# Kernel tuning notes

Measured on AMD Instinct MI355X. Metric: run time of the kernel, lower is better.

The kernel has to match this reference:

```python
import jax, jax.numpy as jnp
import numpy as np

B, L, D = 16, 2048, 192  # batch, frames_per_data, units
H, K = 4, 12             # num_heads, key_dim (hardcoded in build())
EPS = 1e-3               # keras LayerNormalization default epsilon


def layer_norm(x, g, b):
    m = jnp.mean(x, axis=-1, keepdims=True)
    v = jnp.mean(jnp.square(x - m), axis=-1, keepdims=True)
    return (x - m) * jax.lax.rsqrt(v + EPS) * g + b


def conv1d_valid(x, w, b):
    # x: [B,L,C], w: [3,Cin,Cout] -> [B,L-2,Cout]
    return jax.lax.conv_general_dilated(
        x, w, window_strides=(1,), padding='VALID',
        dimension_numbers=('NWC', 'WIO', 'NWC')) + b


def setup_inputs() -> dict:
    key = jax.random.key(0)
    ks = jax.random.split(key, 16)
    s = 0.05
    return {
        'x': jax.random.normal(ks[0], (B, L, D), jnp.float32),
        'ln1_g': jnp.ones((D,), jnp.float32),
        'ln1_b': jnp.zeros((D,), jnp.float32),
        'wq': jax.random.normal(ks[1], (D, H, K), jnp.float32) * s,
        'bq': jnp.zeros((H, K), jnp.float32),
        'wk': jax.random.normal(ks[2], (D, H, K), jnp.float32) * s,
        'bk': jnp.zeros((H, K), jnp.float32),
        'wv': jax.random.normal(ks[3], (D, H, K), jnp.float32) * s,
        'bv': jnp.zeros((H, K), jnp.float32),
        'wo': jax.random.normal(ks[4], (H, K, D), jnp.float32) * s,
        'bo': jnp.zeros((D,), jnp.float32),
        'ln2_g': jnp.ones((D,), jnp.float32),
        'ln2_b': jnp.zeros((D,), jnp.float32),
        'c1_w': jax.random.normal(ks[5], (3, D, D), jnp.float32) * s,
        'c1_b': jnp.zeros((D,), jnp.float32),
        'c2_w': jax.random.normal(ks[6], (3, D, D), jnp.float32) * s,
        'c2_b': jnp.zeros((D,), jnp.float32),
    }


def reference(x, ln1_g, ln1_b, wq, bq, wk, bk, wv, bv, wo, bo,
              ln2_g, ln2_b, c1_w, c1_b, c2_w, c2_b):
    # --- LN1 + causal MHA + residual (dropout = identity at inference) ---
    xn = layer_norm(x, ln1_g, ln1_b)
    q = jnp.einsum('bld,dhk->blhk', xn, wq) + bq
    k = jnp.einsum('bld,dhk->blhk', xn, wk) + bk
    v = jnp.einsum('bld,dhk->blhk', xn, wv) + bv
    scores = jnp.einsum('blhk,bmhk->bhlm', q, k) / jnp.sqrt(jnp.float32(K))
    causal = jnp.tril(jnp.ones((L, L), jnp.float32))  # tril(True) mask
    scores = scores + (1.0 - causal) * (-1e9)          # keras additive mask
    attn = jax.nn.softmax(scores, axis=-1)
    ctx = jnp.einsum('bhlm,bmhk->blhk', attn, v)
    mha = jnp.einsum('blhk,hkd->bld', ctx, wo) + bo
    x = x + mha
    # --- LN2 + positionwise Conv1D feedforward + residual ---
    xn = layer_norm(x, ln2_g, ln2_b)
    h = jax.nn.relu(conv1d_valid(xn, c1_w, c1_b))      # [B,L-2,D]
    h = jnp.pad(h, ((0, 0), (1, 1), (0, 0)))           # ZeroPadding1D(1,1)
    h = conv1d_valid(h, c2_w, c2_b)                    # [B,L-2,D]
    h = jnp.pad(h, ((0, 0), (1, 1), (0, 0)))
    return x + h
```

## Files before the change

### kernel.cpp

```cpp
#include <hip/hip_runtime.h>
#include <hip/hip_bf16.h>

#define L_ 2048
#define D_ 192
#define HK_ 48
#define EPS_ 1e-3f
#define SCALE_ 0.28867513459481287f

typedef __hip_bfloat16 bf16;
typedef _Float16 f16;
typedef __fp16 hf16x2 __attribute__((ext_vector_type(2)));
typedef _Float16 f16x4 __attribute__((ext_vector_type(4)));
typedef __bf16 bf16x8 __attribute__((ext_vector_type(8)));
typedef float  f32x4  __attribute__((ext_vector_type(4)));

__device__ __forceinline__ float b2f(bf16 x) { return __bfloat162float(x); }
__device__ __forceinline__ bf16 f2b(float x) { return __float2bfloat16(x); }

__global__ __launch_bounds__(256) void k_prep_all(
    const float* __restrict__ c1w, const float* __restrict__ c2w,
    const float* __restrict__ wq, const float* __restrict__ wk, const float* __restrict__ wv,
    const float* __restrict__ bq, const float* __restrict__ bk, const float* __restrict__ bv,
    const float* __restrict__ wo,
    bf16* __restrict__ wrep1, bf16* __restrict__ wrep2,
    bf16* __restrict__ wrepq, float* __restrict__ bias144, bf16* __restrict__ wrepo)
{
    const int i = blockIdx.x * 256 + threadIdx.x;
    if (i < 110592) {
        const int k = i / 192, n = i - k * 192;
        wrep1[((size_t)(k >> 5) * 192 + n) * 32 + (k & 31)] = f2b(c1w[i]);
    } else if (i < 221184) {
        const int j = i - 110592;
        const int k = j / 192, n = j - k * 192;
        wrep2[((size_t)(k >> 5) * 192 + n) * 32 + (k & 31)] = f2b(c2w[j]);
    } else if (i < 248832) {
        const int j = i - 221184;
        const int kb = j / 4608, rem = j % 4608;
        const int n = rem / 32, kk = rem % 32;
        const int k = kb * 32 + kk;
        float v;
        if (n < 48)       v = wq[k * HK_ + n] * SCALE_;
        else if (n < 96)  v = wk[k * HK_ + (n - 48)];
        else              v = wv[k * HK_ + (n - 96)];
        wrepq[j] = f2b(v);
    } else if (i < 248976) {
        const int j = i - 248832;
        bias144[j] = (j < 48) ? bq[j] * SCALE_
                   : (j < 96) ? bk[j - 48] : bv[j - 96];
    } else if (i < 261264) {
        const int j = i - 248976;
        const int kb = j / 6144, rem = j % 6144;
        const int n = rem / 32, kk = rem % 32;
        const int k = kb * 32 + kk;
        wrepo[j] = f2b(k < 48 ? wo[k * D_ + n] : 0.f);
    }
}

__global__ __launch_bounds__(256) void k_ln_qkv(
    const float* __restrict__ x, const float* __restrict__ g1, const float* __restrict__ b1,
    const bf16* __restrict__ wrep, const float* __restrict__ bias144,
    f16* __restrict__ qo, f16* __restrict__ ko, f16* __restrict__ vt)
{
    __shared__ bf16 xn[64 * 200];
    const int tid = threadIdx.x;
    const int wave = tid >> 6, lane = tid & 63;
    const int rowbase = blockIdx.x * 64;
    const int b = rowbase >> 11;
    const int lrow0 = rowbase & 2047;

    const float gg0 = g1[lane], gg1 = g1[lane + 64], gg2 = g1[lane + 128];
    const float bb0 = b1[lane], bb1 = b1[lane + 64], bb2 = b1[lane + 128];
    for (int i = 0; i < 16; ++i) {
        const int r = wave * 16 + i;
        const float* xp = x + (size_t)(rowbase + r) * D_;
        const float x0 = xp[lane];
        const float x1 = xp[lane + 64];
        const float x2 = xp[lane + 128];
        float s = x0 + x1 + x2;
        float q = x0 * x0 + x1 * x1 + x2 * x2;
        #pragma unroll
        for (int m = 1; m < 64; m <<= 1) {
            s += __shfl_xor(s, m, 64);
            q += __shfl_xor(q, m, 64);
        }
        const float mean = s * (1.0f / 192.0f);
        const float var  = q * (1.0f / 192.0f) - mean * mean;
        const float rs   = rsqrtf(var + EPS_);
        xn[r * 200 + lane]       = f2b((x0 - mean) * rs * gg0 + bb0);
        xn[r * 200 + lane + 64]  = f2b((x1 - mean) * rs * gg1 + bb1);
        xn[r * 200 + lane + 128] = f2b((x2 - mean) * rs * gg2 + bb2);
    }

    {
        const int h  = tid >> 6;
        const int vc = 12 + ((tid >> 4) & 3);
        const int p0 = lrow0 + (tid & 15) * 4;
        f16x4 vv;
        vv[0] = vv[1] = vv[2] = vv[3] = (vc == 12) ? (f16)1.0f : (f16)0.0f;
        *(f16x4*)(vt + ((size_t)(b * 4 + h) * 16 + vc) * 2048 + p0) = vv;
    }
    __syncthreads();

    const int l15 = lane & 15, q4 = lane >> 4;
    f32x4 acc[9];
    #pragma unroll
    for (int nt = 0; nt < 9; ++nt) acc[nt] = (f32x4){0.f, 0.f, 0.f, 0.f};

    const bf16* xrow = xn + (wave * 16 + l15) * 200 + q4 * 8;
    #pragma unroll
    for (int kb = 0; kb < 6; ++kb) {
        const bf16x8 a = *(const bf16x8*)(xrow + kb * 32);
        const bf16* wp = wrep + ((size_t)kb * 144 + l15) * 32 + q4 * 8;
        #pragma unroll
        for (int nt = 0; nt < 9; ++nt) {
            const bf16x8 bfr = *(const bf16x8*)(wp + (size_t)nt * 16 * 32);
            acc[nt] = __builtin_amdgcn_mfma_f32_16x16x32_bf16(a, bfr, acc[nt], 0, 0, 0);
        }
    }

    const int rw = rowbase + wave * 16 + q4 * 4;
    #pragma unroll
    for (int nt = 0; nt < 9; ++nt) {
        const int col = nt * 16 + l15;
        const float bd = bias144[col];
        if (nt < 3) {
            #pragma unroll
            for (int reg = 0; reg < 4; ++reg)
                qo[(size_t)(rw + reg) * HK_ + col] = (f16)(acc[nt][reg] + bd);
        } else if (nt < 6) {
            #pragma unroll
            for (int reg = 0; reg < 4; ++reg)
                ko[(size_t)(rw + reg) * HK_ + (col - 48)] = (f16)(acc[nt][reg] + bd);
        } else {
            const int vcol = col - 96;
            const int h = vcol / 12, c12 = vcol % 12;
            f16x4 vv;
            #pragma unroll
            for (int reg = 0; reg < 4; ++reg) vv[reg] = (f16)(acc[nt][reg] + bd);
            *(f16x4*)(vt + ((size_t)(b * 4 + h) * 16 + c12) * 2048 +
                      lrow0 + wave * 16 + q4 * 4) = vv;
        }
    }
}

__global__ __launch_bounds__(256) void k_attn_part(
    const f16* __restrict__ qh, const f16* __restrict__ kh, const f16* __restrict__ vt,
    bf16* __restrict__ part_o, float* __restrict__ part_l)
{
    const int tid = threadIdx.x;
    const int wv = tid >> 6, lane = tid & 63;
    const int quad = lane >> 4, l15 = lane & 15;
    const int bh = blockIdx.x / 36;
    int r = blockIdx.x % 36;
    int qt = 0;
    while (r >= qt + 1) { r -= qt + 1; ++qt; }
    const int ks = r;
    const int b = bh >> 2, h = bh & 3;
    const size_t base  = (size_t)b * L_ * HK_ + h * 12;
    const size_t vbase = ((size_t)bh * 16 + l15) * 2048;
    const int kbase = ks * 256;
    const int qbase = qt * 256 + wv * 64;
    const bool diag = (ks == qt);
    const int ktmax = diag ? 4 * (wv + 1) : 16;

    f16x4 Qf[4];
    #pragma unroll
    for (int s = 0; s < 4; ++s) {
        f16x4 v;
        if (quad < 3)
            v = *(const f16x4*)(qh + base + (size_t)(qbase + s * 16 + l15) * HK_ + quad * 4);
        else { v[0] = (f16)1.0f; v[1] = 0; v[2] = 0; v[3] = 0; }
        Qf[s] = v;
    }

    f32x4 O[4];
    #pragma unroll
    for (int s = 0; s < 4; ++s) O[s] = (f32x4){0.f, 0.f, 0.f, 0.f};

    for (int g = 0; g < ktmax; g += 4) {
        f16x4 Kg[4], Vg[4];
        #pragma unroll
        for (int u = 0; u < 4; ++u) {
            const int kt = g + u;
            f16x4 kf;
            if (quad < 3)
                kf = *(const f16x4*)(kh + base + (size_t)(kbase + kt * 16 + l15) * HK_ + quad * 4);
            else { kf[0] = (f16)-6.0f; kf[1] = 0; kf[2] = 0; kf[3] = 0; }
            Kg[u] = kf;
            Vg[u] = *(const f16x4*)(vt + vbase + kbase + kt * 16 + quad * 4);
        }
        #pragma unroll
        for (int u = 0; u < 4; ++u) {
            const int k0 = kbase + (g + u) * 16 + quad * 4;
            #pragma unroll
            for (int s = 0; s < 4; ++s) {
                f32x4 sc = (f32x4){0.f, 0.f, 0.f, 0.f};
                sc = __builtin_amdgcn_mfma_f32_16x16x16f16(Kg[u], Qf[s], sc, 0, 0, 0);
                float p0 = __expf(sc[0]), p1 = __expf(sc[1]);
                float p2 = __expf(sc[2]), p3 = __expf(sc[3]);
                if (diag) {
                    const int qg = qbase + s * 16 + l15;
                    p0 = (k0 + 0 <= qg) ? p0 : 0.f;
                    p1 = (k0 + 1 <= qg) ? p1 : 0.f;
                    p2 = (k0 + 2 <= qg) ? p2 : 0.f;
                    p3 = (k0 + 3 <= qg) ? p3 : 0.f;
                }
                const hf16x2 lo = __builtin_amdgcn_cvt_pkrtz(p0, p1);
                const hf16x2 hi = __builtin_amdgcn_cvt_pkrtz(p2, p3);
                f16x4 p;
                p[0] = (f16)lo[0]; p[1] = (f16)lo[1];
                p[2] = (f16)hi[0]; p[3] = (f16)hi[1];
                O[s] = __builtin_amdgcn_mfma_f32_16x16x16f16(p, Vg[u], O[s], 0, 0, 0);
            }
        }
    }

    const size_t pobase = (size_t)(bh * 8 + ks) * 2048;
    #pragma unroll
    for (int s = 0; s < 4; ++s) {
        const int q16 = qbase + s * 16;
        #pragma unroll
        for (int j = 0; j < 4; ++j) {
            const int qq = q16 + quad * 4 + j;
            if (l15 < 12)       part_o[(pobase + qq) * 12 + l15] = f2b(O[s][j]);
            else if (l15 == 12) part_l[pobase + qq] = O[s][j];
        }
    }
}

__global__ __launch_bounds__(256) void k_proj_ln2(
    const float* __restrict__ x, const bf16* __restrict__ part_o,
    const float* __restrict__ part_l, const bf16* __restrict__ wrepo,
    const float* __restrict__ bo, const float* __restrict__ g2,
    const float* __restrict__ lb2, bf16* __restrict__ x2b,
    bf16* __restrict__ xn2b)
{
    __shared__ bf16 ct[64 * 72];
    const int tid = threadIdx.x;
    const int wave = tid >> 6, lane = tid & 63;
    const int rowbase = blockIdx.x * 64;
    const int b = rowbase >> 11, lrow = rowbase & 2047;
    const int ns = (lrow >> 8) + 1;

    {
        const int rr = tid >> 2, h = tid & 3;
        const int q = lrow + rr;
        const bf16* op = part_o + ((size_t)(b * 4 + h) * 8 * 2048 + q) * 12;
        const float* lp = part_l + (size_t)(b * 4 + h) * 8 * 2048 + q;
        float o[12];
        #pragma unroll
        for (int i = 0; i < 12; ++i) o[i] = 0.f;
        float l = 0.f;
        for (int s = 0; s < ns; ++s) {
            l += lp[(size_t)s * 2048];
            #pragma unroll
            for (int i = 0; i < 12; ++i) o[i] += b2f(op[(size_t)s * 2048 * 12 + i]);
        }
        const float inv = 1.0f / l;
        #pragma unroll
        for (int i = 0; i < 12; ++i) ct[rr * 72 + h * 12 + i] = f2b(o[i] * inv);
        const int c0 = 48 + h * 4;
        #pragma unroll
        for (int i = 0; i < 4; ++i) ct[rr * 72 + c0 + i] = f2b(0.f);
    }
    __syncthreads();

    const int l15 = lane & 15, q4 = lane >> 4;
    f32x4 acc[12];
    #pragma unroll
    for (int nt = 0; nt < 12; ++nt) acc[nt] = (f32x4){0.f, 0.f, 0.f, 0.f};
    const bf16* arow = ct + (wave * 16 + l15) * 72 + q4 * 8;
    #pragma unroll
    for (int kb = 0; kb < 2; ++kb) {
        const bf16x8 a = *(const bf16x8*)(arow + kb * 32);
        const bf16* wp = wrepo + ((size_t)kb * 192 + l15) * 32 + q4 * 8;
        #pragma unroll
        for (int nt = 0; nt < 12; ++nt) {
            const bf16x8 bb = *(const bf16x8*)(wp + (size_t)nt * 16 * 32);
            acc[nt] = __builtin_amdgcn_mfma_f32_16x16x32_bf16(a, bb, acc[nt], 0, 0, 0);
        }
    }

    const int rw0 = rowbase + wave * 16 + q4 * 4;
    float sum[4] = {0.f, 0.f, 0.f, 0.f}, ssum[4] = {0.f, 0.f, 0.f, 0.f};
    #pragma unroll
    for (int nt = 0; nt < 12; ++nt) {
        const int col = nt * 16 + l15;
        const float bod = bo[col];
        #pragma unroll
        for (int reg = 0; reg < 4; ++reg) {
            const float v = acc[nt][reg] + bod + x[(size_t)(rw0 + reg) * D_ + col];
            acc[nt][reg] = v;
            x2b[(size_t)(rw0 + reg) * D_ + col] = f2b(v);
            sum[reg] += v; ssum[reg] += v * v;
        }
    }
    #pragma unroll
    for (int m = 1; m <= 8; m <<= 1) {
        #pragma unroll
        for (int reg = 0; reg < 4; ++reg) {
            sum[reg]  += __shfl_xor(sum[reg], m, 64);
            ssum[reg] += __shfl_xor(ssum[reg], m, 64);
        }
    }
    float mean[4], rs[4];
    #pragma unroll
    for (int reg = 0; reg < 4; ++reg) {
        mean[reg] = sum[reg] * (1.0f / 192.0f);
        const float var = ssum[reg] * (1.0f / 192.0f) - mean[reg] * mean[reg];
        rs[reg] = rsqrtf(var + EPS_);
    }
    #pragma unroll
    for (int nt = 0; nt < 12; ++nt) {
        const int col = nt * 16 + l15;
        const float g = g2[col], bb2 = lb2[col];
        #pragma unroll
        for (int reg = 0; reg < 4; ++reg)
            xn2b[(size_t)(rw0 + reg) * D_ + col] =
                f2b((acc[nt][reg] - mean[reg]) * rs[reg] * g + bb2);
    }
}

#define INROWB 400
#define HTOFF  27200
__global__ __launch_bounds__(256, 2) void k_conv_fused(
    const bf16* __restrict__ act, const bf16* __restrict__ w1,
    const float* __restrict__ b1c, const bf16* __restrict__ w2,
    const float* __restrict__ b2c, const bf16* __restrict__ x2b,
    float* __restrict__ outf)
{
    __shared__ __align__(16) char lds[27200 + 26400];

    const int tid = threadIdx.x;
    const int wave = tid >> 6, lane = tid & 63;
    const int m16 = lane & 15, q = lane >> 4;
    const int rowbase = blockIdx.x * 64;
    const int lrow = rowbase & (L_ - 1);

    {
        const bf16* src0 = act + ((long long)rowbase - 2) * D_;
        bf16x8 v[7];
        int dst[7];
        #pragma unroll
        for (int i = 0; i < 7; ++i) {
            const int g = tid + i * 256;
            if (g < 1632) {
                v[i] = *(const bf16x8*)(src0 + g * 8);
                const int row = (g * 2731) >> 16;
                dst[i] = row * INROWB + (g - row * 24) * 16;
            }
        }
        #pragma unroll
        for (int i = 0; i < 7; ++i) {
            const int g = tid + i * 256;
            if (g < 1632) *(bf16x8*)(lds + dst[i]) = v[i];
        }
    }

    const int laneA = m16 * INROWB + q * 16;
    const int colw = wave * 48;
    float bd1[3], bd2[3];
    #pragma unroll
    for (int j = 0; j < 3; ++j) {
        bd1[j] = b1c[colw + j * 16 + m16];
        bd2[j] = b2c[colw + j * 16 + m16];
    }
    __syncthreads();

    f32x4 acc1[5][3];
    #pragma unroll
    for (int mt = 0; mt < 5; ++mt)
        #pragma unroll
        for (int j = 0; j < 3; ++j) acc1[mt][j] = (f32x4){0.f, 0.f, 0.f, 0.f};

    #define LOADB(w, kb, j) \
        (*(const bf16x8*)((w) + ((size_t)(kb) * 192 + m16) * 32 + q * 8 \
                          + (size_t)(wave * 3 + (j)) * 16 * 32))
    {
        bf16x8 bB[2][3];
        #pragma unroll
        for (int j = 0; j < 3; ++j) bB[0][j] = LOADB(w1, 0, j);
        #pragma unroll
        for (int kb = 0; kb < 18; ++kb) {
            if (kb + 1 < 18) {
                #pragma unroll
                for (int j = 0; j < 3; ++j) bB[(kb + 1) & 1][j] = LOADB(w1, kb + 1, j);
            }
            const int t = kb / 6, c6 = kb % 6;
            bf16x8 a[5];
            #pragma unroll
            for (int mt = 0; mt < 5; ++mt)
                a[mt] = *(const bf16x8*)(lds + laneA + (mt * 16 + t) * INROWB + c6 * 64);
            #pragma unroll
            for (int j = 0; j < 3; ++j)
                #pragma unroll
                for (int mt = 0; mt < 5; ++mt)
                    acc1[mt][j] = __builtin_amdgcn_mfma_f32_16x16x32_bf16(
                        a[mt], bB[kb & 1][j], acc1[mt][j], 0, 0, 0);
        }
    }

    #pragma unroll
    for (int mt = 0; mt < 5; ++mt)
        #pragma unroll
        for (int j = 0; j < 3; ++j)
            #pragma unroll
            for (int reg = 0; reg < 4; ++reg) {
                const int hr = mt * 16 + q * 4 + reg;
                if (hr < 66) {
                    const int hm = lrow + hr - 1;
                    float v = fmaxf(acc1[mt][j][reg] + bd1[j], 0.f);
                    if (hm == 0 || hm == L_ - 1) v = 0.f;
                    *(bf16*)(lds + HTOFF + hr * INROWB + (colw + j * 16 + m16) * 2) = f2b(v);
                }
            }
    __syncthreads();

    float xr[3][4][4];
    #pragma unroll
    for (int j = 0; j < 3; ++j)
        #pragma unroll
        for (int mt = 0; mt < 4; ++mt)
            #pragma unroll
            for (int reg = 0; reg < 4; ++reg)
                xr[j][mt][reg] = b2f(x2b[(size_t)(rowbase + mt * 16 + q * 4 + reg) * D_
                                         + colw + j * 16 + m16]);

    f32x4 acc2[4][3];
    #pragma unroll
    for (int mt = 0; mt < 4; ++mt)
        #pragma unroll
        for (int j = 0; j < 3; ++j) acc2[mt][j] = (f32x4){0.f, 0.f, 0.f, 0.f};
    {
        bf16x8 bB[2][3];
        #pragma unroll
        for (int j = 0; j < 3; ++j) bB[0][j] = LOADB(w2, 0, j);
        #pragma unroll
        for (int kb = 0; kb < 18; ++kb) {
            if (kb + 1 < 18) {
                #pragma unroll
                for (int j = 0; j < 3; ++j) bB[(kb + 1) & 1][j] = LOADB(w2, kb + 1, j);
            }
            const int t = kb / 6, c6 = kb % 6;
            bf16x8 a[4];
            #pragma unroll
            for (int mt = 0; mt < 4; ++mt)
                a[mt] = *(const bf16x8*)(lds + HTOFF + laneA + (mt * 16 + t) * INROWB + c6 * 64);
            #pragma unroll
            for (int j = 0; j < 3; ++j)
                #pragma unroll
                for (int mt = 0; mt < 4; ++mt)
                    acc2[mt][j] = __builtin_amdgcn_mfma_f32_16x16x32_bf16(
                        a[mt], bB[kb & 1][j], acc2[mt][j], 0, 0, 0);
        }
    }
    #undef LOADB

    #pragma unroll
    for (int j = 0; j < 3; ++j)
        #pragma unroll
        for (int mt = 0; mt < 4; ++mt)
            #pragma unroll
            for (int reg = 0; reg < 4; ++reg) {
                const int r = rowbase + mt * 16 + q * 4 + reg;
                const int m = r & (L_ - 1);
                float v = xr[j][mt][reg];
                if (m != 0 && m != L_ - 1) v += acc2[mt][j][reg] + bd2[j];
                outf[(size_t)r * D_ + colw + j * 16 + m16] = v;
            }
}

extern "C" void kernel_launch(void* const* d_in, const int* in_sizes, int n_in,
                              void* d_out, int out_size, void* d_ws, size_t ws_size,
                              hipStream_t stream)
{
    const float* x    = (const float*)d_in[0];
    const float* ln1g = (const float*)d_in[1];
    const float* ln1b = (const float*)d_in[2];
    const float* wq   = (const float*)d_in[3];
    const float* bq   = (const float*)d_in[4];
    const float* wk   = (const float*)d_in[5];
    const float* bk   = (const float*)d_in[6];
    const float* wv   = (const float*)d_in[7];
    const float* bv   = (const float*)d_in[8];
    const float* wo   = (const float*)d_in[9];
    const float* bo   = (const float*)d_in[10];
    const float* ln2g = (const float*)d_in[11];
    const float* ln2b = (const float*)d_in[12];
    const float* c1w  = (const float*)d_in[13];
    const float* c1b  = (const float*)d_in[14];
    const float* c2w  = (const float*)d_in[15];
    const float* c2b  = (const float*)d_in[16];

    const size_t ROWS = (size_t)16 * L_;
    char* ws = (char*)d_ws;
    size_t off = 4096;
    bf16* xn2b = (bf16*)(ws + off); off += ROWS * D_ * 2;
    off += 4096;
    bf16* hpb  = (bf16*)(ws + off); off += ROWS * D_ * 2;
    off += 4096;
    bf16* x2b  = (bf16*)(ws + off); off += ROWS * D_ * 2;
    f16* qb    = (f16*)(ws + off);   off += ROWS * HK_ * 2;
    f16* kb    = (f16*)(ws + off);   off += ROWS * HK_ * 2;
    f16* vt    = (f16*)(ws + off);   off += (size_t)64 * 16 * 2048 * 2;
    bf16* part_o = (bf16*)(ws + off); off += (size_t)64 * 8 * 2048 * 12 * 2;
    float* part_l = (float*)(ws + off); off += (size_t)64 * 8 * 2048 * 4;
    bf16* wrep1 = (bf16*)(ws + off); off += 576 * 192 * 2;
    bf16* wrep2 = (bf16*)(ws + off); off += 576 * 192 * 2;
    bf16* wrepq = (bf16*)(ws + off); off += 6 * 144 * 32 * 2;
    float* bias144 = (float*)(ws + off); off += 144 * 4;
    bf16* wrepo = (bf16*)(ws + off); off += 2 * 192 * 32 * 2;

    (void)hpb;
    k_prep_all   <<<1021, 256, 0, stream>>>(c1w, c2w, wq, wk, wv, bq, bk, bv, wo,
                                            wrep1, wrep2, wrepq, bias144, wrepo);
    k_ln_qkv     <<< 512, 256, 0, stream>>>(x, ln1g, ln1b, wrepq, bias144, qb, kb, vt);
    k_attn_part  <<<64 * 36, 256, 0, stream>>>(qb, kb, vt, part_o, part_l);
    k_proj_ln2   <<< 512, 256, 0, stream>>>(x, part_o, part_l, wrepo, bo, ln2g, ln2b,
                                            x2b, xn2b);
    k_conv_fused <<< 512, 256, 0, stream>>>(xn2b, wrep1, c1b, wrep2, c2b, x2b,
                                            (float*)d_out);
}
```

Measured before the change: 202.1 us.

## Halve row tiles per block, split columns across waves, use exp2 in attention

The LN/QKV, projection+LN2 and fused conv kernels now process 32 rows per block instead of 64 and launch twice as many blocks. Where needed, waves split the output columns, and LN2 partial sums are combined through shared memory. Attention folds log2(e) into the Q scaling and the shift term so it can call the hardware exp2 directly, and its K-tile unroll drops from 4 to 2, with higher launch-bound occupancy hints. The aim is more parallelism and occupancy across the 256 CUs, at the cost of more conv halo recompute (36 input rows per 32 outputs) and an extra block barrier.

Measured after the change: 194.3 us. -3.9%, faster.

```diff
diff --git a/kernel.cpp b/kernel.cpp
--- a/kernel.cpp
+++ b/kernel.cpp
@@ -6,6 +6,7 @@
 #define HK_ 48
 #define EPS_ 1e-3f
 #define SCALE_ 0.28867513459481287f
+#define LOG2E_ 1.4426950408889634f
 
 typedef __hip_bfloat16 bf16;
 typedef _Float16 f16;
@@ -39,13 +40,13 @@
         const int n = rem / 32, kk = rem % 32;
         const int k = kb * 32 + kk;
         float v;
-        if (n < 48)       v = wq[k * HK_ + n] * SCALE_;
+        if (n < 48)       v = wq[k * HK_ + n] * (SCALE_ * LOG2E_);
         else if (n < 96)  v = wk[k * HK_ + (n - 48)];
         else              v = wv[k * HK_ + (n - 96)];
         wrepq[j] = f2b(v);
     } else if (i < 248976) {
         const int j = i - 248832;
-        bias144[j] = (j < 48) ? bq[j] * SCALE_
+        bias144[j] = (j < 48) ? bq[j] * (SCALE_ * LOG2E_)
                    : (j < 96) ? bk[j - 48] : bv[j - 96];
     } else if (i < 261264) {
         const int j = i - 248976;
@@ -56,22 +57,22 @@
     }
 }
 
-__global__ __launch_bounds__(256) void k_ln_qkv(
+__global__ __launch_bounds__(256, 4) void k_ln_qkv(
     const float* __restrict__ x, const float* __restrict__ g1, const float* __restrict__ b1,
     const bf16* __restrict__ wrep, const float* __restrict__ bias144,
     f16* __restrict__ qo, f16* __restrict__ ko, f16* __restrict__ vt)
 {
-    __shared__ bf16 xn[64 * 200];
+    __shared__ bf16 xn[32 * 200];
     const int tid = threadIdx.x;
     const int wave = tid >> 6, lane = tid & 63;
-    const int rowbase = blockIdx.x * 64;
+    const int rowbase = blockIdx.x * 32;
     const int b = rowbase >> 11;
     const int lrow0 = rowbase & 2047;
 
     const float gg0 = g1[lane], gg1 = g1[lane + 64], gg2 = g1[lane + 128];
     const float bb0 = b1[lane], bb1 = b1[lane + 64], bb2 = b1[lane + 128];
-    for (int i = 0; i < 16; ++i) {
-        const int r = wave * 16 + i;
+    for (int i = 0; i < 8; ++i) {
+        const int r = wave * 8 + i;
         const float* xp = x + (size_t)(rowbase + r) * D_;
         const float x0 = xp[lane];
         const float x1 = xp[lane + 64];
@@ -91,10 +92,10 @@
         xn[r * 200 + lane + 128] = f2b((x2 - mean) * rs * gg2 + bb2);
     }
 
-    {
-        const int h  = tid >> 6;
-        const int vc = 12 + ((tid >> 4) & 3);
-        const int p0 = lrow0 + (tid & 15) * 4;
+    if (tid < 128) {
+        const int h  = tid >> 5;
+        const int vc = 12 + ((tid >> 3) & 3);
+        const int p0 = lrow0 + (tid & 7) * 4;
         f16x4 vv;
         vv[0] = vv[1] = vv[2] = vv[3] = (vc == 12) ? (f16)1.0f : (f16)0.0f;
         *(f16x4*)(vt + ((size_t)(b * 4 + h) * 16 + vc) * 2048 + p0) = vv;
@@ -102,48 +103,56 @@
     __syncthreads();
 
     const int l15 = lane & 15, q4 = lane >> 4;
-    f32x4 acc[9];
-    #pragma unroll
-    for (int nt = 0; nt < 9; ++nt) acc[nt] = (f32x4){0.f, 0.f, 0.f, 0.f};
-
-    const bf16* xrow = xn + (wave * 16 + l15) * 200 + q4 * 8;
+    const int rt = wave >> 1, g = wave & 1;
+    const int ntlim = 5 - g;
+    f32x4 acc[5];
+    #pragma unroll
+    for (int nt = 0; nt < 5; ++nt) acc[nt] = (f32x4){0.f, 0.f, 0.f, 0.f};
+
+    const bf16* xrow = xn + (rt * 16 + l15) * 200 + q4 * 8;
     #pragma unroll
     for (int kb = 0; kb < 6; ++kb) {
         const bf16x8 a = *(const bf16x8*)(xrow + kb * 32);
-        const bf16* wp = wrep + ((size_t)kb * 144 + l15) * 32 + q4 * 8;
-        #pragma unroll
-        for (int nt = 0; nt < 9; ++nt) {
-            const bf16x8 bfr = *(const bf16x8*)(wp + (size_t)nt * 16 * 32);
-            acc[nt] = __builtin_amdgcn_mfma_f32_16x16x32_bf16(a, bfr, acc[nt], 0, 0, 0);
-        }
-    }
-
-    const int rw = rowbase + wave * 16 + q4 * 4;
-    #pragma unroll
-    for (int nt = 0; nt < 9; ++nt) {
-        const int col = nt * 16 + l15;
-        const float bd = bias144[col];
-        if (nt < 3) {
-            #pragma unroll
-            for (int reg = 0; reg < 4; ++reg)
-                qo[(size_t)(rw + reg) * HK_ + col] = (f16)(acc[nt][reg] + bd);
-        } else if (nt < 6) {
-            #pragma unroll
-            for (int reg = 0; reg < 4; ++reg)
-                ko[(size_t)(rw + reg) * HK_ + (col - 48)] = (f16)(acc[nt][reg] + bd);
-        } else {
-            const int vcol = col - 96;
-            const int h = vcol / 12, c12 = vcol % 12;
-            f16x4 vv;
-            #pragma unroll
-            for (int reg = 0; reg < 4; ++reg) vv[reg] = (f16)(acc[nt][reg] + bd);
-            *(f16x4*)(vt + ((size_t)(b * 4 + h) * 16 + c12) * 2048 +
-                      lrow0 + wave * 16 + q4 * 4) = vv;
+        const bf16* wp = wrep + ((size_t)kb * 144 + l15) * 32 + q4 * 8
+                       + (size_t)(g * 5) * 16 * 32;
+        #pragma unroll
+        for (int nt = 0; nt < 5; ++nt) {
+            if (nt < ntlim) {
+                const bf16x8 bfr = *(const bf16x8*)(wp + (size_t)nt * 16 * 32);
+                acc[nt] = __builtin_amdgcn_mfma_f32_16x16x32_bf16(a, bfr, acc[nt], 0, 0, 0);
+            }
+        }
+    }
+
+    const int rw = rowbase + rt * 16 + q4 * 4;
+    #pragma unroll
+    for (int nt = 0; nt < 5; ++nt) {
+        if (nt < ntlim) {
+            const int ntg = g * 5 + nt;
+            const int col = ntg * 16 + l15;
+            const float bd = bias144[col];
+            if (ntg < 3) {
+                #pragma unroll
+                for (int reg = 0; reg < 4; ++reg)
+                    qo[(size_t)(rw + reg) * HK_ + col] = (f16)(acc[nt][reg] + bd);
+            } else if (ntg < 6) {
+                #pragma unroll
+                for (int reg = 0; reg < 4; ++reg)
+                    ko[(size_t)(rw + reg) * HK_ + (col - 48)] = (f16)(acc[nt][reg] + bd);
+            } else {
+                const int vcol = col - 96;
+                const int h = vcol / 12, c12 = vcol % 12;
+                f16x4 vv;
+                #pragma unroll
+                for (int reg = 0; reg < 4; ++reg) vv[reg] = (f16)(acc[nt][reg] + bd);
+                *(f16x4*)(vt + ((size_t)(b * 4 + h) * 16 + c12) * 2048 +
+                          lrow0 + rt * 16 + q4 * 4) = vv;
+            }
         }
     }
 }
 
-__global__ __launch_bounds__(256) void k_attn_part(
+__global__ __launch_bounds__(256, 8) void k_attn_part(
     const f16* __restrict__ qh, const f16* __restrict__ kh, const f16* __restrict__ vt,
     bf16* __restrict__ part_o, float* __restrict__ part_l)
 {
@@ -169,7 +178,7 @@
         f16x4 v;
         if (quad < 3)
             v = *(const f16x4*)(qh + base + (size_t)(qbase + s * 16 + l15) * HK_ + quad * 4);
-        else { v[0] = (f16)1.0f; v[1] = 0; v[2] = 0; v[3] = 0; }
+        else { v[0] = (f16)LOG2E_; v[1] = 0; v[2] = 0; v[3] = 0; }
         Qf[s] = v;
     }
 
@@ -177,10 +186,10 @@
     #pragma unroll
     for (int s = 0; s < 4; ++s) O[s] = (f32x4){0.f, 0.f, 0.f, 0.f};
 
-    for (int g = 0; g < ktmax; g += 4) {
-        f16x4 Kg[4], Vg[4];
-        #pragma unroll
-        for (int u = 0; u < 4; ++u) {
+    for (int g = 0; g < ktmax; g += 2) {
+        f16x4 Kg[2], Vg[2];
+        #pragma unroll
+        for (int u = 0; u < 2; ++u) {
             const int kt = g + u;
             f16x4 kf;
             if (quad < 3)
@@ -190,14 +199,16 @@
             Vg[u] = *(const f16x4*)(vt + vbase + kbase + kt * 16 + quad * 4);
         }
         #pragma unroll
-        for (int u = 0; u < 4; ++u) {
+        for (int u = 0; u < 2; ++u) {
             const int k0 = kbase + (g + u) * 16 + quad * 4;
             #pragma unroll
             for (int s = 0; s < 4; ++s) {
                 f32x4 sc = (f32x4){0.f, 0.f, 0.f, 0.f};
                 sc = __builtin_amdgcn_mfma_f32_16x16x16f16(Kg[u], Qf[s], sc, 0, 0, 0);
-                float p0 = __expf(sc[0]), p1 = __expf(sc[1]);
-                float p2 = __expf(sc[2]), p3 = __expf(sc[3]);
+                float p0 = __builtin_amdgcn_exp2f(sc[0]);
+                float p1 = __builtin_amdgcn_exp2f(sc[1]);
+                float p2 = __builtin_amdgcn_exp2f(sc[2]);
+                float p3 = __builtin_amdgcn_exp2f(sc[3]);
                 if (diag) {
                     const int qg = qbase + s * 16 + l15;
                     p0 = (k0 + 0 <= qg) ? p0 : 0.f;
@@ -228,21 +239,22 @@
     }
 }
 
-__global__ __launch_bounds__(256) void k_proj_ln2(
+__global__ __launch_bounds__(256, 4) void k_proj_ln2(
     const float* __restrict__ x, const bf16* __restrict__ part_o,
     const float* __restrict__ part_l, const bf16* __restrict__ wrepo,
     const float* __restrict__ bo, const float* __restrict__ g2,
     const float* __restrict__ lb2, bf16* __restrict__ x2b,
     bf16* __restrict__ xn2b)
 {
-    __shared__ bf16 ct[64 * 72];
+    __shared__ bf16 ct[32 * 72];
+    __shared__ float psum[4][4][4][2];
     const int tid = threadIdx.x;
     const int wave = tid >> 6, lane = tid & 63;
-    const int rowbase = blockIdx.x * 64;
+    const int rowbase = blockIdx.x * 32;
     const int b = rowbase >> 11, lrow = rowbase & 2047;
     const int ns = (lrow >> 8) + 1;
 
-    {
+    if (tid < 128) {
         const int rr = tid >> 2, h = tid & 3;
         const int q = lrow + rr;
         const bf16* op = part_o + ((size_t)(b * 4 + h) * 8 * 2048 + q) * 12;
@@ -266,31 +278,33 @@
     __syncthreads();
 
     const int l15 = lane & 15, q4 = lane >> 4;
-    f32x4 acc[12];
-    #pragma unroll
-    for (int nt = 0; nt < 12; ++nt) acc[nt] = (f32x4){0.f, 0.f, 0.f, 0.f};
-    const bf16* arow = ct + (wave * 16 + l15) * 72 + q4 * 8;
+    const int rt = wave >> 1, g = wave & 1;
+    f32x4 acc[6];
+    #pragma unroll
+    for (int j = 0; j < 6; ++j) acc[j] = (f32x4){0.f, 0.f, 0.f, 0.f};
+    const bf16* arow = ct + (rt * 16 + l15) * 72 + q4 * 8;
     #pragma unroll
     for (int kb = 0; kb < 2; ++kb) {
         const bf16x8 a = *(const bf16x8*)(arow + kb * 32);
-        const bf16* wp = wrepo + ((size_t)kb * 192 + l15) * 32 + q4 * 8;
-        #pragma unroll
-        for (int nt = 0; nt < 12; ++nt) {
-            const bf16x8 bb = *(const bf16x8*)(wp + (size_t)nt * 16 * 32);
-            acc[nt] = __builtin_amdgcn_mfma_f32_16x16x32_bf16(a, bb, acc[nt], 0, 0, 0);
-        }
-    }
-
-    const int rw0 = rowbase + wave * 16 + q4 * 4;
+        const bf16* wp = wrepo + ((size_t)kb * 192 + l15) * 32 + q4 * 8
+                       + (size_t)(g * 6) * 16 * 32;
+        #pragma unroll
+        for (int j = 0; j < 6; ++j) {
+            const bf16x8 bb = *(const bf16x8*)(wp + (size_t)j * 16 * 32);
+            acc[j] = __builtin_amdgcn_mfma_f32_16x16x32_bf16(a, bb, acc[j], 0, 0, 0);
+        }
+    }
+
+    const int rw0 = rowbase + rt * 16 + q4 * 4;
     float sum[4] = {0.f, 0.f, 0.f, 0.f}, ssum[4] = {0.f, 0.f, 0.f, 0.f};
     #pragma unroll
-    for (int nt = 0; nt < 12; ++nt) {
-        const int col = nt * 16 + l15;
+    for (int j = 0; j < 6; ++j) {
+        const int col = (g * 6 + j) * 16 + l15;
         const float bod = bo[col];
         #pragma unroll
         for (int reg = 0; reg < 4; ++reg) {
-            const float v = acc[nt][reg] + bod + x[(size_t)(rw0 + reg) * D_ + col];
-            acc[nt][reg] = v;
+            const float v = acc[j][reg] + bod + x[(size_t)(rw0 + reg) * D_ + col];
+            acc[j][reg] = v;
             x2b[(size_t)(rw0 + reg) * D_ + col] = f2b(v);
             sum[reg] += v; ssum[reg] += v * v;
         }
@@ -303,57 +317,69 @@
             ssum[reg] += __shfl_xor(ssum[reg], m, 64);
         }
     }
+    if (l15 == 0) {
+        #pragma unroll
+        for (int reg = 0; reg < 4; ++reg) {
+            psum[wave][q4][reg][0] = sum[reg];
+            psum[wave][q4][reg][1] = ssum[reg];
+        }
+    }
+    __syncthreads();
     float mean[4], rs[4];
     #pragma unroll
     for (int reg = 0; reg < 4; ++reg) {
-        mean[reg] = sum[reg] * (1.0f / 192.0f);
-        const float var = ssum[reg] * (1.0f / 192.0f) - mean[reg] * mean[reg];
+        const float st = sum[reg]  + psum[wave ^ 1][q4][reg][0];
+        const float qt2 = ssum[reg] + psum[wave ^ 1][q4][reg][1];
+        mean[reg] = st * (1.0f / 192.0f);
+        const float var = qt2 * (1.0f / 192.0f) - mean[reg] * mean[reg];
         rs[reg] = rsqrtf(var + EPS_);
     }
     #pragma unroll
-    for (int nt = 0; nt < 12; ++nt) {
-        const int col = nt * 16 + l15;
-        const float g = g2[col], bb2 = lb2[col];
+    for (int j = 0; j < 6; ++j) {
+        const int col = (g * 6 + j) * 16 + l15;
+        const float gg = g2[col], bb2 = lb2[col];
         #pragma unroll
         for (int reg = 0; reg < 4; ++reg)
             xn2b[(size_t)(rw0 + reg) * D_ + col] =
-                f2b((acc[nt][reg] - mean[reg]) * rs[reg] * g + bb2);
+                f2b((acc[j][reg] - mean[reg]) * rs[reg] * gg + bb2);
     }
 }
 
 #define INROWB 400
-#define HTOFF  27200
-__global__ __launch_bounds__(256, 2) void k_conv_fused(
+#define NIN    36
+#define NH     34
+#define HTOFF  (NIN * INROWB)
+__global__ __launch_bounds__(256, 4) void k_conv_fused(
     const bf16* __restrict__ act, const bf16* __restrict__ w1,
     const float* __restrict__ b1c, const bf16* __restrict__ w2,
     const float* __restrict__ b2c, const bf16* __restrict__ x2b,
     float* __restrict__ outf)
 {
-    __shared__ __align__(16) char lds[27200 + 26400];
+    __shared__ __align__(16) char lds[NIN * INROWB + NH * INROWB];
 
     const int tid = threadIdx.x;
     const int wave = tid >> 6, lane = tid & 63;
     const int m16 = lane & 15, q = lane >> 4;
-    const int rowbase = blockIdx.x * 64;
+    const int rowbase = blockIdx.x * 32;
     const int lrow = rowbase & (L_ - 1);
 
     {
         const bf16* src0 = act + ((long long)rowbase - 2) * D_;
-        bf16x8 v[7];
-        int dst[7];
-        #pragma unroll
-        for (int i = 0; i < 7; ++i) {
+        bf16x8 v[4];
+        int dst[4];
+        #pragma unroll
+        for (int i = 0; i < 4; ++i) {
             const int g = tid + i * 256;
-            if (g < 1632) {
+            if (g < 864) {
                 v[i] = *(const bf16x8*)(src0 + g * 8);
                 const int row = (g * 2731) >> 16;
                 dst[i] = row * INROWB + (g - row * 24) * 16;
             }
         }
         #pragma unroll
-        for (int i = 0; i < 7; ++i) {
+        for (int i = 0; i < 4; ++i) {
             const int g = tid + i * 256;
-            if (g < 1632) *(bf16x8*)(lds + dst[i]) = v[i];
+            if (g < 864) *(bf16x8*)(lds + dst[i]) = v[i];
         }
     }
 
@@ -367,9 +393,9 @@
     }
     __syncthreads();
 
-    f32x4 acc1[5][3];
-    #pragma unroll
-    for (int mt = 0; mt < 5; ++mt)
+    f32x4 acc1[3][3];
+    #pragma unroll
+    for (int mt = 0; mt < 3; ++mt)
         #pragma unroll
         for (int j = 0; j < 3; ++j) acc1[mt][j] = (f32x4){0.f, 0.f, 0.f, 0.f};
 
@@ -387,48 +413,48 @@
                 for (int j = 0; j < 3; ++j) bB[(kb + 1) & 1][j] = LOADB(w1, kb + 1, j);
             }
             const int t = kb / 6, c6 = kb % 6;
-            bf16x8 a[5];
-            #pragma unroll
-            for (int mt = 0; mt < 5; ++mt)
+            bf16x8 a[3];
+            #pragma unroll
+            for (int mt = 0; mt < 3; ++mt)
                 a[mt] = *(const bf16x8*)(lds + laneA + (mt * 16 + t) * INROWB + c6 * 64);
             #pragma unroll
             for (int j = 0; j < 3; ++j)
                 #pragma unroll
-                for (int mt = 0; mt < 5; ++mt)
+                for (int mt = 0; mt < 3; ++mt)
                     acc1[mt][j] = __builtin_amdgcn_mfma_f32_16x16x32_bf16(
                         a[mt], bB[kb & 1][j], acc1[mt][j], 0, 0, 0);
         }
     }
 
     #pragma unroll
-    for (int mt = 0; mt < 5; ++mt)
+    for (int mt = 0; mt < 3; ++mt)
         #pragma unroll
         for (int j = 0; j < 3; ++j)
             #pragma unroll
             for (int reg = 0; reg < 4; ++reg) {
                 const int hr = mt * 16 + q * 4 + reg;
-                if (hr < 66) {
+                if (hr < NH) {
                     const int hm = lrow + hr - 1;
                     float v = fmaxf(acc1[mt][j][reg] + bd1[j], 0.f);
                     if (hm == 0 || hm == L_ - 1) v = 0.f;
                     *(bf16*)(lds + HTOFF + hr * INROWB + (colw + j * 16 + m16) * 2) = f2b(v);
                 }
             }
-    __syncthreads();
-
-    float xr[3][4][4];
+
+    float xr[3][2][4];
     #pragma unroll
     for (int j = 0; j < 3; ++j)
         #pragma unroll
-        for (int mt = 0; mt < 4; ++mt)
+        for (int mt = 0; mt < 2; ++mt)
             #pragma unroll
             for (int reg = 0; reg < 4; ++reg)
                 xr[j][mt][reg] = b2f(x2b[(size_t)(rowbase + mt * 16 + q * 4 + reg) * D_
                                          + colw + j * 16 + m16]);
-
-    f32x4 acc2[4][3];
-    #pragma unroll
-    for (int mt = 0; mt < 4; ++mt)
+    __syncthreads();
+
+    f32x4 acc2[2][3];
+    #pragma unroll
+    for (int mt = 0; mt < 2; ++mt)
         #pragma unroll
         for (int j = 0; j < 3; ++j) acc2[mt][j] = (f32x4){0.f, 0.f, 0.f, 0.f};
     {
@@ -442,14 +468,14 @@
                 for (int j = 0; j < 3; ++j) bB[(kb + 1) & 1][j] = LOADB(w2, kb + 1, j);
             }
             const int t = kb / 6, c6 = kb % 6;
-            bf16x8 a[4];
-            #pragma unroll
-            for (int mt = 0; mt < 4; ++mt)
+            bf16x8 a[2];
+            #pragma unroll
+            for (int mt = 0; mt < 2; ++mt)
                 a[mt] = *(const bf16x8*)(lds + HTOFF + laneA + (mt * 16 + t) * INROWB + c6 * 64);
             #pragma unroll
             for (int j = 0; j < 3; ++j)
                 #pragma unroll
-                for (int mt = 0; mt < 4; ++mt)
+                for (int mt = 0; mt < 2; ++mt)
                     acc2[mt][j] = __builtin_amdgcn_mfma_f32_16x16x32_bf16(
                         a[mt], bB[kb & 1][j], acc2[mt][j], 0, 0, 0);
         }
@@ -459,7 +485,7 @@
     #pragma unroll
     for (int j = 0; j < 3; ++j)
         #pragma unroll
-        for (int mt = 0; mt < 4; ++mt)
+        for (int mt = 0; mt < 2; ++mt)
             #pragma unroll
             for (int reg = 0; reg < 4; ++reg) {
                 const int r = rowbase + mt * 16 + q * 4 + reg;
@@ -514,10 +540,10 @@
     (void)hpb;
     k_prep_all   <<<1021, 256, 0, stream>>>(c1w, c2w, wq, wk, wv, bq, bk, bv, wo,
                                             wrep1, wrep2, wrepq, bias144, wrepo);
-    k_ln_qkv     <<< 512, 256, 0, stream>>>(x, ln1g, ln1b, wrepq, bias144, qb, kb, vt);
+    k_ln_qkv     <<<1024, 256, 0, stream>>>(x, ln1g, ln1b, wrepq, bias144, qb, kb, vt);
     k_attn_part  <<<64 * 36, 256, 0, stream>>>(qb, kb, vt, part_o, part_l);
-    k_proj_ln2   <<< 512, 256, 0, stream>>>(x, part_o, part_l, wrepo, bo, ln2g, ln2b,
+    k_proj_ln2   <<<1024, 256, 0, stream>>>(x, part_o, part_l, wrepo, bo, ln2g, ln2b,
                                             x2b, xn2b);
-    k_conv_fused <<< 512, 256, 0, stream>>>(xn2b, wrep1, c1b, wrep2, c2b, x2b,
+    k_conv_fused <<<1024, 256, 0, stream>>>(xn2b, wrep1, c1b, wrep2, c2b, x2b,
                                             (float*)d_out);
 }
```
